# Performance work log

Measured on AMD Instinct MI355X. Metric: run time of the kernel, lower is better.

Reference implementation:

```python
import jax, jax.numpy as jnp
import numpy as np
from jax import lax

B, N, C = 16, 2048, 128
NPOINT = 512
RADII = (0.1, 0.2, 0.4)
NSAMPLES = (16, 32, 48)
C_IN = C + 3          # use_xyz: relative xyz concatenated to features
C_OUT = 128
C_MID = C_OUT // 4    # mapping_func1 out channels (non-first-layer)


def fps(xyz, npoint):
    # sequential furthest point sampling; first index is 0 (matches CUDA FPS)
    b, n, _ = xyz.shape
    def step(carry, _):
        dist, last = carry
        p = xyz[jnp.arange(b), last]                    # (B,3) last selected point
        d = jnp.sum((xyz - p[:, None, :]) ** 2, -1)     # (B,N)
        dist = jnp.minimum(dist, d)
        nxt = jnp.argmax(dist, -1).astype(jnp.int32)
        return (dist, nxt), nxt
    idx0 = jnp.zeros((b,), jnp.int32)
    (_, _), rest = lax.scan(step, (jnp.full((b, n), 1e10, jnp.float32), idx0), None, length=npoint - 1)
    return jnp.concatenate([idx0[None], rest], 0).T     # (B,npoint)


def ball_query(xyz, new_xyz, radius, nsample):
    # first `nsample` in-ball indices (in original point order), pad with first hit
    n = xyz.shape[1]
    d2 = jnp.sum((new_xyz[:, :, None, :] - xyz[:, None, :, :]) ** 2, -1)  # (B,np,N)
    scores = jnp.where(d2 < radius * radius, jnp.arange(n, dtype=jnp.int32), n)
    vals = -lax.top_k(-scores, nsample)[0]               # ascending valid indices, invalid == n
    first = vals[..., :1]                                # center is always in its own ball
    return jnp.where(vals >= n, first, vals)             # (B,np,ns) int32


def gather_points(pts, idx):
    # pts (B,N,D), idx (B,np,ns) -> (B,np,ns,D)
    return jax.vmap(lambda p, i: p[i])(pts, idx)


def sa_forward(xyz, features, W1, b1, W2, b2, Wcr, bcr):
    fi = fps(xyz, NPOINT)
    new_xyz = jax.vmap(lambda p, i: p[i])(xyz, fi)       # (B,np,3)
    featT = jnp.transpose(features, (0, 2, 1))           # (B,N,C)
    outs = []
    for r, ns in zip(RADII, NSAMPLES):
        idx = ball_query(xyz, new_xyz, r, ns)
        g_xyz = gather_points(xyz, idx)                  # (B,np,ns,3) absolute neighbor coords
        rel = g_xyz - new_xyz[:, :, None, :]             # relative coords
        gf = gather_points(featT, idx)                   # (B,np,ns,C)
        x = jnp.concatenate([rel, gf], -1)               # (B,np,ns,C_in)
        dist = jnp.linalg.norm(rel, axis=-1, keepdims=True)
        ci = jnp.broadcast_to(new_xyz[:, :, None, :], g_xyz.shape)
        h10 = jnp.concatenate([dist, ci, g_xyz, rel], -1)        # relation prior (B,np,ns,10)
        h = jax.nn.relu(h10 @ W1 + b1) @ W2 + b2                 # dynamic weights (B,np,ns,C_in)
        pooled = jnp.max(jax.nn.relu(h * x), 2)                  # (B,np,C_in) max over neighbors
        outs.append(jax.nn.relu(pooled @ Wcr + bcr))             # channel raising (B,np,C_out)
    new_features = jnp.transpose(jnp.concatenate(outs, -1), (0, 2, 1))  # (B, 3*C_out, np)
    return new_xyz, new_features


def setup_inputs() -> dict:
    key = jax.random.key(0)
    ks = jax.random.split(key, 6)
    s = 0.05
    xyz = jax.random.uniform(ks[0], (B, N, 3), jnp.float32)
    features = jax.random.normal(ks[1], (B, C, N), jnp.float32)
    W1 = jax.random.normal(ks[2], (10, C_MID), jnp.float32) * s
    b1 = jnp.zeros((C_MID,), jnp.float32)
    W2 = jax.random.normal(ks[3], (C_MID, C_IN), jnp.float32) * s
    b2 = jnp.zeros((C_IN,), jnp.float32)
    Wcr = jax.random.normal(ks[4], (C_IN, C_OUT), jnp.float32) * s
    bcr = jnp.zeros((C_OUT,), jnp.float32)
    return dict(xyz=xyz, features=features, W1=W1, b1=b1, W2=W2, b2=b2, Wcr=Wcr, bcr=bcr)


def reference(xyz, features, W1, b1, W2, b2, Wcr, bcr):
    return sa_forward(xyz, features, W1, b1, W2, b2, Wcr, bcr)
```

## Files before the change

kernel.cpp:

```cpp
#include <hip/hip_runtime.h>
#include <hip/hip_bf16.h>

#define BATCH   16
#define NPTS    2048
#define NPOINT  512
#define CFEAT   128
#define CIN     131
#define CMID    32

typedef _Float16 half8 __attribute__((ext_vector_type(8)));
typedef float floatx4 __attribute__((ext_vector_type(4)));

__device__ __forceinline__ float d2_rn(float ax, float ay, float az,
                                       float bx, float by, float bz) {
  float dx = __fsub_rn(ax, bx), dy = __fsub_rn(ay, by), dz = __fsub_rn(az, bz);
  return __fadd_rn(__fadd_rn(__fmul_rn(dx, dx), __fmul_rn(dy, dy)), __fmul_rn(dz, dz));
}

__device__ __forceinline__ void wave_key_reduce(unsigned &hi, unsigned &lo) {
#define KSTEP(CTRL, RM, BM) {                                                     \
    unsigned h2 = (unsigned)__builtin_amdgcn_update_dpp((int)hi, (int)hi, CTRL,   \
                                                        RM, BM, false);           \
    unsigned l2 = (unsigned)__builtin_amdgcn_update_dpp((int)lo, (int)lo, CTRL,   \
                                                        RM, BM, false);           \
    bool g = (h2 > hi) || (h2 == hi && l2 > lo);                                  \
    hi = g ? h2 : hi; lo = g ? l2 : lo; }
  KSTEP(0x111, 0xf, 0xf)
  KSTEP(0x112, 0xf, 0xf)
  KSTEP(0x114, 0xf, 0xe)
  KSTEP(0x118, 0xf, 0xc)
  KSTEP(0x142, 0xa, 0xf)
  KSTEP(0x143, 0xc, 0xf)
#undef KSTEP
}

__global__ __launch_bounds__(256, 1) void fps_transpose_kernel(
    const float* __restrict__ xyz, const float* __restrict__ feat,
    float* __restrict__ featT, float* __restrict__ out_xyz)
{
  int t = threadIdx.x;
  if (blockIdx.x >= BATCH) {
    __shared__ float tile[32][33];
    int m  = blockIdx.x - BATCH;
    int b  = m >> 8;
    int c0 = ((m >> 6) & 3) << 5;
    int n0 = (m & 63) << 5;
    int tx = t & 31, ty = t >> 5;
    const float* src = feat  + (size_t)b * CFEAT * NPTS;
    float*       dst = featT + (size_t)b * NPTS * CFEAT;
#pragma unroll
    for (int i = 0; i < 4; ++i)
      tile[ty + 8 * i][tx] = src[(size_t)(c0 + ty + 8 * i) * NPTS + n0 + tx];
    __syncthreads();
#pragma unroll
    for (int i = 0; i < 4; ++i)
      dst[(size_t)(n0 + ty + 8 * i) * CFEAT + c0 + tx] = tile[tx][ty + 8 * i];
    return;
  }
  __shared__ float4 sp[NPTS];
  __shared__ unsigned long long skey[2][4];
  int b = blockIdx.x, lane = t & 63, wid = t >> 6;
  const float* xb = xyz + (size_t)b * NPTS * 3;
  for (int n = t; n < NPTS; n += 256) {
    const float* p = xb + n * 3;
    sp[n] = make_float4(p[0], p[1], p[2], 0.f);
  }
  __syncthreads();
  float px[8], py[8], pz[8], d[8];
#pragma unroll
  for (int i = 0; i < 8; ++i) {
    float4 q = sp[(i << 8) + t];
    px[i] = q.x; py[i] = q.y; pz[i] = q.z;
    d[i] = 1e10f;
  }
  float cx, cy, cz;
  { float4 q = sp[0]; cx = q.x; cy = q.y; cz = q.z; }
  if (t == 0) {
    float* o = out_xyz + (size_t)b * NPOINT * 3;
    o[0] = cx; o[1] = cy; o[2] = cz;
  }
#pragma unroll 1
  for (int step = 1; step < NPOINT; ++step) {
    unsigned long long bk = 0ull;
#pragma unroll
    for (int i = 0; i < 8; ++i) {
      float dd = d2_rn(px[i], py[i], pz[i], cx, cy, cz);
      float nd = fminf(d[i], dd);
      d[i] = nd;
      unsigned long long key = ((unsigned long long)__float_as_uint(nd) << 32)
                             | (unsigned)~((i << 8) + t);
      bk = key > bk ? key : bk;
    }
    unsigned khi = (unsigned)(bk >> 32), klo = (unsigned)bk;
    wave_key_reduce(khi, klo);
    int p = step & 1;
    if (lane == 63)
      skey[p][wid] = ((unsigned long long)khi << 32) | (unsigned long long)klo;
    __syncthreads();
    unsigned long long k0 = skey[p][0], k1 = skey[p][1];
    unsigned long long k2 = skey[p][2], k3 = skey[p][3];
    unsigned long long ka = k0 > k1 ? k0 : k1;
    unsigned long long kb = k2 > k3 ? k2 : k3;
    unsigned long long km = ka > kb ? ka : kb;
    int last = (int)(~(unsigned)(km & 0xFFFFFFFFull)) & (NPTS - 1);
    float4 q = sp[last];
    cx = q.x; cy = q.y; cz = q.z;
    if (t == 0) {
      float* o = out_xyz + ((size_t)b * NPOINT + step) * 3;
      o[0] = cx; o[1] = cy; o[2] = cz;
    }
  }
}

__global__ __launch_bounds__(256) void center_kernel(
    const float* __restrict__ xyz, const float* __restrict__ featT,
    const float* __restrict__ W1, const float* __restrict__ b1,
    const float* __restrict__ W2, const float* __restrict__ b2,
    const float* __restrict__ Wcr, const float* __restrict__ bcr,
    const float* __restrict__ new_xyz, float* __restrict__ out_feat)
{
  int j = blockIdx.x, b = blockIdx.y, t = threadIdx.x;
  int wid = t >> 6, lane = t & 63;
  int quad = lane >> 4, col = lane & 15;
  __shared__ _Float16 sW2T[144][40];
  __shared__ _Float16 sH1T[96][40];
  __shared__ float sRel[96][4];
  __shared__ int   sIdx[96];
  __shared__ int   lI0[4][16], lI1[4][32], lI2[4][48];
  __shared__ int   lC[4][3];
  __shared__ float sPool[3][132];

  for (int i = t; i < 144 * 32; i += 256) {
    int m = i >> 5, k = i & 31;
    float v = (m < CIN) ? W2[k * CIN + m] : 0.f;
    sW2T[m][k] = (_Float16)v;
  }
  float cx = new_xyz[((size_t)b * NPOINT + j) * 3 + 0];
  float cy = new_xyz[((size_t)b * NPOINT + j) * 3 + 1];
  float cz = new_xyz[((size_t)b * NPOINT + j) * 3 + 2];
  {
    const float* xb = xyz + (size_t)b * NPTS * 3;
    unsigned long long lt = (1ull << lane) - 1ull;
    int c0 = 0, c1 = 0, c2 = 0;
    for (int it = 0; it < 8; ++it) {
      int n = (wid << 9) + (it << 6) + lane;
      float qx = xb[n * 3 + 0], qy = xb[n * 3 + 1], qz = xb[n * 3 + 2];
      float d2 = d2_rn(cx, cy, cz, qx, qy, qz);
      bool i0 = d2 < 0.01f, i1 = d2 < 0.04f, i2 = d2 < 0.16f;
      unsigned long long m0 = __ballot(i0), m1 = __ballot(i1), m2 = __ballot(i2);
      if (i0) { int p = c0 + __popcll(m0 & lt); if (p < 16) lI0[wid][p] = n; }
      if (i1) { int p = c1 + __popcll(m1 & lt); if (p < 32) lI1[wid][p] = n; }
      if (i2) { int p = c2 + __popcll(m2 & lt); if (p < 48) lI2[wid][p] = n; }
      c0 += __popcll(m0); c1 += __popcll(m1); c2 += __popcll(m2);
    }
    if (lane == 0) { lC[wid][0] = c0; lC[wid][1] = c1; lC[wid][2] = c2; }
  }
  __syncthreads();

  if (t < 96) {
    int rad = (t < 16) ? 0 : ((t < 48) ? 1 : 2);
    int g = t - ((rad == 0) ? 0 : ((rad == 1) ? 16 : 48));
    int q0 = lC[0][rad], q1 = lC[1][rad], q2 = lC[2][rad], q3 = lC[3][rad];
    const int* L0 = (rad == 0) ? lI0[0] : (rad == 1) ? lI1[0] : lI2[0];
    const int* L1 = (rad == 0) ? lI0[1] : (rad == 1) ? lI1[1] : lI2[1];
    const int* L2 = (rad == 0) ? lI0[2] : (rad == 1) ? lI1[2] : lI2[2];
    const int* L3 = (rad == 0) ? lI0[3] : (rad == 1) ? lI1[3] : lI2[3];
    int idx = -1, gg = g;
    if (gg < q0) idx = L0[gg]; else { gg -= q0;
    if (gg < q1) idx = L1[gg]; else { gg -= q1;
    if (gg < q2) idx = L2[gg]; else { gg -= q2;
    if (gg < q3) idx = L3[gg]; } } }
    if (idx < 0)
      idx = (q0 > 0) ? L0[0] : (q1 > 0) ? L1[0] : (q2 > 0) ? L2[0] : L3[0];
    sIdx[t] = idx;

    const float* pp = xyz + ((size_t)b * NPTS + (size_t)idx) * 3;
    float ppx = pp[0], ppy = pp[1], ppz = pp[2];
    float rx = __fsub_rn(ppx, cx), ry = __fsub_rn(ppy, cy), rz = __fsub_rn(ppz, cz);
    float dist = sqrtf(__fadd_rn(__fadd_rn(__fmul_rn(rx, rx), __fmul_rn(ry, ry)),
                                 __fmul_rn(rz, rz)));
    sRel[t][0] = rx; sRel[t][1] = ry; sRel[t][2] = rz; sRel[t][3] = 0.f;
    float h10[10] = {dist, cx, cy, cz, ppx, ppy, ppz, rx, ry, rz};
    _Float16 h1h[CMID];
#pragma unroll
    for (int k = 0; k < CMID; ++k) {
      float a = b1[k];
#pragma unroll
      for (int i = 0; i < 10; ++i) a = fmaf(h10[i], W1[i * CMID + k], a);
      h1h[k] = (_Float16)fmaxf(a, 0.f);
    }
    uint4* dstv = (uint4*)&sH1T[t][0];
    const uint4* srcv = (const uint4*)h1h;
#pragma unroll
    for (int q = 0; q < 4; ++q) dstv[q] = srcv[q];
  }
  __syncthreads();

  const float* ftb = featT + (size_t)b * NPTS * CFEAT;
#pragma unroll 1
  for (int nt = wid; nt < 9; nt += 4) {
    int c = (nt << 4) + col;
    half8 Bv = *(const half8*)&sW2T[c][quad << 3];
    float b2c = (c < CIN) ? b2[c] : 0.f;
    float sm0 = 0.f, sm1 = 0.f, sm2 = 0.f;
#pragma unroll
    for (int mt = 0; mt < 6; ++mt) {
      half8 A = *(const half8*)&sH1T[(mt << 4) + col][quad << 3];
      floatx4 acc = {0.f, 0.f, 0.f, 0.f};
      acc = __builtin_amdgcn_mfma_f32_16x16x32_f16(A, Bv, acc, 0, 0, 0);
#pragma unroll
      for (int r = 0; r < 4; ++r) {
        int sm = (mt << 4) + (quad << 2) + r;
        float x;
        if (c < 3)        x = sRel[sm][c];
        else if (c < CIN) x = ftb[(size_t)sIdx[sm] * CFEAT + (c - 3)];
        else              x = 0.f;
        float h2 = __fadd_rn(acc[r], b2c);
        float v = fmaxf(__fmul_rn(h2, x), 0.f);
        if (mt == 0)      sm0 = fmaxf(sm0, v);
        else if (mt < 3)  sm1 = fmaxf(sm1, v);
        else              sm2 = fmaxf(sm2, v);
      }
    }
    sm0 = fmaxf(sm0, __shfl_xor(sm0, 16)); sm0 = fmaxf(sm0, __shfl_xor(sm0, 32));
    sm1 = fmaxf(sm1, __shfl_xor(sm1, 16)); sm1 = fmaxf(sm1, __shfl_xor(sm1, 32));
    sm2 = fmaxf(sm2, __shfl_xor(sm2, 16)); sm2 = fmaxf(sm2, __shfl_xor(sm2, 32));
    if (quad == 0 && c < CIN) {
      sPool[0][c] = sm0; sPool[1][c] = sm1; sPool[2][c] = sm2;
    }
  }
  __syncthreads();

  if (t < CFEAT) {
    float s0 = bcr[t], s1 = s0, s2 = s0;
#pragma unroll 4
    for (int k = 0; k < CIN; ++k) {
      float w = Wcr[k * CFEAT + t];
      s0 = fmaf(sPool[0][k], w, s0);
      s1 = fmaf(sPool[1][k], w, s1);
      s2 = fmaf(sPool[2][k], w, s2);
    }
    float* ob = out_feat + (size_t)b * 384 * NPOINT + j;
    ob[(size_t)(0 * CFEAT + t) * NPOINT] = fmaxf(s0, 0.f);
    ob[(size_t)(1 * CFEAT + t) * NPOINT] = fmaxf(s1, 0.f);
    ob[(size_t)(2 * CFEAT + t) * NPOINT] = fmaxf(s2, 0.f);
  }
}

extern "C" void kernel_launch(void* const* d_in, const int* in_sizes, int n_in,
                              void* d_out, int out_size, void* d_ws, size_t ws_size,
                              hipStream_t stream) {
  const float* xyz  = (const float*)d_in[0];
  const float* feat = (const float*)d_in[1];
  const float* W1   = (const float*)d_in[2];
  const float* b1   = (const float*)d_in[3];
  const float* W2   = (const float*)d_in[4];
  const float* b2   = (const float*)d_in[5];
  const float* Wcr  = (const float*)d_in[6];
  const float* bcr  = (const float*)d_in[7];
  float* out_xyz  = (float*)d_out;
  float* out_feat = out_xyz + (size_t)BATCH * NPOINT * 3;
  float* featT    = (float*)d_ws;

  fps_transpose_kernel<<<BATCH + BATCH * 256, 256, 0, stream>>>(xyz, feat, featT, out_xyz);
  center_kernel<<<dim3(NPOINT, BATCH), 256, 0, stream>>>(
      xyz, featT, W1, b1, W2, b2, Wcr, bcr, (const float*)d_out, out_feat);
}
```

Before: 580.6 us.

## Process two FPS batches per block and restructure center kernel loads and output

The FPS part now handles two batch elements per block, interleaving their independent distance updates and reductions so one block's latency-bound loop does twice the work with half the barriers per batch. Selected centers are buffered in shared memory and written out once at the end instead of per step. The center kernel swaps grid dimensions so blocks of the same point index across batches are scheduled together. It also transposes W2 with coalesced per-thread loads, caches b2 in shared memory, and spreads the channel-raising matmul over all 256 threads instead of 128. The FPS change doubles register and LDS use per block and keeps the sequential chain length the same.

New measurement: 836.7 us. 1.44x slower.

```diff
diff --git a/kernel.cpp b/kernel.cpp
--- a/kernel.cpp
+++ b/kernel.cpp
@@ -7,6 +7,7 @@
 #define CFEAT   128
 #define CIN     131
 #define CMID    32
+#define NFPSBLK 8
 
 typedef _Float16 half8 __attribute__((ext_vector_type(8)));
 typedef float floatx4 __attribute__((ext_vector_type(4)));
@@ -39,9 +40,9 @@
     float* __restrict__ featT, float* __restrict__ out_xyz)
 {
   int t = threadIdx.x;
-  if (blockIdx.x >= BATCH) {
+  if (blockIdx.x >= NFPSBLK) {
     __shared__ float tile[32][33];
-    int m  = blockIdx.x - BATCH;
+    int m  = blockIdx.x - NFPSBLK;
     int b  = m >> 8;
     int c0 = ((m >> 6) & 3) << 5;
     int n0 = (m & 63) << 5;
@@ -57,59 +58,91 @@
       dst[(size_t)(n0 + ty + 8 * i) * CFEAT + c0 + tx] = tile[tx][ty + 8 * i];
     return;
   }
-  __shared__ float4 sp[NPTS];
-  __shared__ unsigned long long skey[2][4];
-  int b = blockIdx.x, lane = t & 63, wid = t >> 6;
-  const float* xb = xyz + (size_t)b * NPTS * 3;
+  __shared__ float4 spA[NPTS], spB[NPTS];
+  __shared__ unsigned long long skA[2][4], skB[2][4];
+  __shared__ float scA[NPOINT * 3], scB[NPOINT * 3];
+  int b0 = blockIdx.x * 2, b1 = b0 + 1;
+  int lane = t & 63, wid = t >> 6;
+  const float* xa = xyz + (size_t)b0 * NPTS * 3;
+  const float* xb = xyz + (size_t)b1 * NPTS * 3;
   for (int n = t; n < NPTS; n += 256) {
-    const float* p = xb + n * 3;
-    sp[n] = make_float4(p[0], p[1], p[2], 0.f);
-  }
-  __syncthreads();
-  float px[8], py[8], pz[8], d[8];
+    spA[n] = make_float4(xa[n * 3 + 0], xa[n * 3 + 1], xa[n * 3 + 2], 0.f);
+    spB[n] = make_float4(xb[n * 3 + 0], xb[n * 3 + 1], xb[n * 3 + 2], 0.f);
+  }
+  __syncthreads();
+  float pxA[8], pyA[8], pzA[8], dA[8];
+  float pxB[8], pyB[8], pzB[8], dB[8];
 #pragma unroll
   for (int i = 0; i < 8; ++i) {
-    float4 q = sp[(i << 8) + t];
-    px[i] = q.x; py[i] = q.y; pz[i] = q.z;
-    d[i] = 1e10f;
-  }
-  float cx, cy, cz;
-  { float4 q = sp[0]; cx = q.x; cy = q.y; cz = q.z; }
+    float4 qa = spA[(i << 8) + t];
+    pxA[i] = qa.x; pyA[i] = qa.y; pzA[i] = qa.z; dA[i] = 1e10f;
+    float4 qb = spB[(i << 8) + t];
+    pxB[i] = qb.x; pyB[i] = qb.y; pzB[i] = qb.z; dB[i] = 1e10f;
+  }
+  float cxA, cyA, czA, cxB, cyB, czB;
+  { float4 q = spA[0]; cxA = q.x; cyA = q.y; czA = q.z; }
+  { float4 q = spB[0]; cxB = q.x; cyB = q.y; czB = q.z; }
   if (t == 0) {
-    float* o = out_xyz + (size_t)b * NPOINT * 3;
-    o[0] = cx; o[1] = cy; o[2] = cz;
+    scA[0] = cxA; scA[1] = cyA; scA[2] = czA;
+    scB[0] = cxB; scB[1] = cyB; scB[2] = czB;
   }
 #pragma unroll 1
   for (int step = 1; step < NPOINT; ++step) {
-    unsigned long long bk = 0ull;
+    unsigned long long bkA = 0ull, bkB = 0ull;
 #pragma unroll
     for (int i = 0; i < 8; ++i) {
-      float dd = d2_rn(px[i], py[i], pz[i], cx, cy, cz);
-      float nd = fminf(d[i], dd);
-      d[i] = nd;
-      unsigned long long key = ((unsigned long long)__float_as_uint(nd) << 32)
-                             | (unsigned)~((i << 8) + t);
-      bk = key > bk ? key : bk;
-    }
-    unsigned khi = (unsigned)(bk >> 32), klo = (unsigned)bk;
-    wave_key_reduce(khi, klo);
+      float ddA = d2_rn(pxA[i], pyA[i], pzA[i], cxA, cyA, czA);
+      float ndA = fminf(dA[i], ddA);
+      dA[i] = ndA;
+      unsigned long long keyA = ((unsigned long long)__float_as_uint(ndA) << 32)
+                              | (unsigned)~((i << 8) + t);
+      bkA = keyA > bkA ? keyA : bkA;
+      float ddB = d2_rn(pxB[i], pyB[i], pzB[i], cxB, cyB, czB);
+      float ndB = fminf(dB[i], ddB);
+      dB[i] = ndB;
+      unsigned long long keyB = ((unsigned long long)__float_as_uint(ndB) << 32)
+                              | (unsigned)~((i << 8) + t);
+      bkB = keyB > bkB ? keyB : bkB;
+    }
+    unsigned hA = (unsigned)(bkA >> 32), lA = (unsigned)bkA;
+    unsigned hB = (unsigned)(bkB >> 32), lB = (unsigned)bkB;
+    wave_key_reduce(hA, lA);
+    wave_key_reduce(hB, lB);
     int p = step & 1;
-    if (lane == 63)
-      skey[p][wid] = ((unsigned long long)khi << 32) | (unsigned long long)klo;
+    if (lane == 63) {
+      skA[p][wid] = ((unsigned long long)hA << 32) | (unsigned long long)lA;
+      skB[p][wid] = ((unsigned long long)hB << 32) | (unsigned long long)lB;
+    }
     __syncthreads();
-    unsigned long long k0 = skey[p][0], k1 = skey[p][1];
-    unsigned long long k2 = skey[p][2], k3 = skey[p][3];
-    unsigned long long ka = k0 > k1 ? k0 : k1;
-    unsigned long long kb = k2 > k3 ? k2 : k3;
-    unsigned long long km = ka > kb ? ka : kb;
-    int last = (int)(~(unsigned)(km & 0xFFFFFFFFull)) & (NPTS - 1);
-    float4 q = sp[last];
-    cx = q.x; cy = q.y; cz = q.z;
+    {
+      unsigned long long k0 = skA[p][0], k1 = skA[p][1];
+      unsigned long long k2 = skA[p][2], k3 = skA[p][3];
+      unsigned long long ka = k0 > k1 ? k0 : k1;
+      unsigned long long kb = k2 > k3 ? k2 : k3;
+      unsigned long long km = ka > kb ? ka : kb;
+      int last = (int)(~(unsigned)(km & 0xFFFFFFFFull)) & (NPTS - 1);
+      float4 q = spA[last];
+      cxA = q.x; cyA = q.y; czA = q.z;
+    }
+    {
+      unsigned long long k0 = skB[p][0], k1 = skB[p][1];
+      unsigned long long k2 = skB[p][2], k3 = skB[p][3];
+      unsigned long long ka = k0 > k1 ? k0 : k1;
+      unsigned long long kb = k2 > k3 ? k2 : k3;
+      unsigned long long km = ka > kb ? ka : kb;
+      int last = (int)(~(unsigned)(km & 0xFFFFFFFFull)) & (NPTS - 1);
+      float4 q = spB[last];
+      cxB = q.x; cyB = q.y; czB = q.z;
+    }
     if (t == 0) {
-      float* o = out_xyz + ((size_t)b * NPOINT + step) * 3;
-      o[0] = cx; o[1] = cy; o[2] = cz;
-    }
-  }
+      scA[step * 3 + 0] = cxA; scA[step * 3 + 1] = cyA; scA[step * 3 + 2] = czA;
+      scB[step * 3 + 0] = cxB; scB[step * 3 + 1] = cyB; scB[step * 3 + 2] = czB;
+    }
+  }
+  __syncthreads();
+  float* oA = out_xyz + (size_t)b0 * NPOINT * 3;
+  float* oB = out_xyz + (size_t)b1 * NPOINT * 3;
+  for (int i = t; i < NPOINT * 3; i += 256) { oA[i] = scA[i]; oB[i] = scB[i]; }
 }
 
 __global__ __launch_bounds__(256) void center_kernel(
@@ -119,21 +152,27 @@
     const float* __restrict__ Wcr, const float* __restrict__ bcr,
     const float* __restrict__ new_xyz, float* __restrict__ out_feat)
 {
-  int j = blockIdx.x, b = blockIdx.y, t = threadIdx.x;
+  int b = blockIdx.x, j = blockIdx.y, t = threadIdx.x;
   int wid = t >> 6, lane = t & 63;
   int quad = lane >> 4, col = lane & 15;
   __shared__ _Float16 sW2T[144][40];
   __shared__ _Float16 sH1T[96][40];
+  __shared__ float sB2[144];
   __shared__ float sRel[96][4];
   __shared__ int   sIdx[96];
   __shared__ int   lI0[4][16], lI1[4][32], lI2[4][48];
   __shared__ int   lC[4][3];
   __shared__ float sPool[3][132];
 
-  for (int i = t; i < 144 * 32; i += 256) {
-    int m = i >> 5, k = i & 31;
-    float v = (m < CIN) ? W2[k * CIN + m] : 0.f;
-    sW2T[m][k] = (_Float16)v;
+  {
+    bool act = t < 144;
+    float v;
+#pragma unroll 4
+    for (int k = 0; k < 32; ++k) {
+      v = (t < CIN) ? W2[k * CIN + t] : 0.f;
+      if (act) sW2T[t][k] = (_Float16)v;
+    }
+    if (t < 144) sB2[t] = (t < CIN) ? b2[t] : 0.f;
   }
   float cx = new_xyz[((size_t)b * NPOINT + j) * 3 + 0];
   float cy = new_xyz[((size_t)b * NPOINT + j) * 3 + 1];
@@ -201,7 +240,7 @@
   for (int nt = wid; nt < 9; nt += 4) {
     int c = (nt << 4) + col;
     half8 Bv = *(const half8*)&sW2T[c][quad << 3];
-    float b2c = (c < CIN) ? b2[c] : 0.f;
+    float b2c = sB2[c];
     float sm0 = 0.f, sm1 = 0.f, sm2 = 0.f;
 #pragma unroll
     for (int mt = 0; mt < 6; ++mt) {
@@ -231,19 +270,17 @@
   }
   __syncthreads();
 
-  if (t < CFEAT) {
-    float s0 = bcr[t], s1 = s0, s2 = s0;
+  {
+    float* ob = out_feat + (size_t)b * 384 * NPOINT + j;
+#pragma unroll 1
+    for (int o = t; o < 384; o += 256) {
+      int rad = o >> 7, c = o & 127;
+      const float* pool = sPool[rad];
+      float s = bcr[c];
 #pragma unroll 4
-    for (int k = 0; k < CIN; ++k) {
-      float w = Wcr[k * CFEAT + t];
-      s0 = fmaf(sPool[0][k], w, s0);
-      s1 = fmaf(sPool[1][k], w, s1);
-      s2 = fmaf(sPool[2][k], w, s2);
-    }
-    float* ob = out_feat + (size_t)b * 384 * NPOINT + j;
-    ob[(size_t)(0 * CFEAT + t) * NPOINT] = fmaxf(s0, 0.f);
-    ob[(size_t)(1 * CFEAT + t) * NPOINT] = fmaxf(s1, 0.f);
-    ob[(size_t)(2 * CFEAT + t) * NPOINT] = fmaxf(s2, 0.f);
+      for (int k = 0; k < CIN; ++k) s = fmaf(pool[k], Wcr[k * CFEAT + c], s);
+      ob[(size_t)o * NPOINT] = fmaxf(s, 0.f);
+    }
   }
 }
 
@@ -262,7 +299,7 @@
   float* out_feat = out_xyz + (size_t)BATCH * NPOINT * 3;
   float* featT    = (float*)d_ws;
 
-  fps_transpose_kernel<<<BATCH + BATCH * 256, 256, 0, stream>>>(xyz, feat, featT, out_xyz);
-  center_kernel<<<dim3(NPOINT, BATCH), 256, 0, stream>>>(
+  fps_transpose_kernel<<<NFPSBLK + BATCH * 256, 256, 0, stream>>>(xyz, feat, featT, out_xyz);
+  center_kernel<<<dim3(BATCH, NPOINT), 256, 0, stream>>>(
       xyz, featT, W1, b1, W2, b2, Wcr, bcr, (const float*)d_out, out_feat);
 }
```
